# Kernel optimization log

Measured on AMD Instinct MI355X. Metric: run time of the kernel, lower is better.

Reference implementation:

```python
import jax, jax.numpy as jnp
import numpy as np

N_DELAYS = 512
N_SAMPLES = 2 ** 15  # 32768


def _interp_linear(x, out_size):
    # F.interpolate(mode='linear', align_corners=False) on [B, C, L]
    L = x.shape[-1]
    scale = L / out_size
    pos = (jnp.arange(out_size, dtype=jnp.float32) + 0.5) * scale - 0.5
    pos = jnp.clip(pos, 0.0, L - 1)
    i0 = jnp.floor(pos).astype(jnp.int32)
    i1 = jnp.minimum(i0 + 1, L - 1)
    w = (pos - i0).astype(x.dtype)
    return x[..., i0] * (1.0 - w) + x[..., i1] * w


def _interp_nearest(x, out_size):
    # F.interpolate(mode='nearest') on [B, C, L]: idx = floor(j * L/out)
    L = x.shape[-1]
    idx = jnp.clip(jnp.floor(jnp.arange(out_size) * (L / out_size)).astype(jnp.int32), 0, L - 1)
    return x[..., idx]


def setup_inputs() -> dict:
    key = jax.random.key(0)
    k1, k2, k3, k4, k5 = jax.random.split(key, 5)
    batch = 8
    impulse = jax.random.normal(k1, (batch, 128), dtype=jnp.float32)
    delay_selection = jax.random.normal(k2, (batch, N_DELAYS, 16), dtype=jnp.float32)
    damping = jax.random.normal(k3, (batch, 1), dtype=jnp.float32)
    filt = jax.random.normal(k4, (batch, 16), dtype=jnp.float32)
    # torch forward draws uniform(-1,1) noise; passed as input for determinism
    noise = jax.random.uniform(k5, (batch, 1, N_SAMPLES), dtype=jnp.float32, minval=-1.0, maxval=1.0)
    # comb-filter buffer: delays[i, ::i+1] = 1
    delays_np = np.zeros((N_DELAYS, N_SAMPLES), dtype=np.float32)
    for i in range(N_DELAYS):
        delays_np[i, ::i + 1] = 1.0
    delays = jnp.asarray(delays_np)
    return {"impulse": impulse, "delay_selection": delay_selection, "damping": damping,
            "filt": filt, "noise": noise, "delays": delays}


def reference(impulse, delay_selection, damping, filt, noise, delays):
    batch = delay_selection.shape[0]
    n_delays, n_samples = delays.shape
    n_frames = filt.shape[-1]

    # filter spectrum envelope: sigmoid -> linear upsample to n_samples//2 -> pad 1
    f = jax.nn.sigmoid(filt).reshape(-1, 1, n_frames)
    f = _interp_linear(f, n_samples // 2)
    filt_spec = jnp.pad(f, ((0, 0), (0, 0), (0, 1)))  # [B,1,n_samples//2+1]

    # impulse: squared envelope upsampled, modulating uniform noise
    imp = impulse.reshape(batch, 1, -1) ** 2
    imp = _interp_linear(imp, n_samples) * noise  # [B,1,n_samples]

    # damping: powers = linspace(1, 1, n_frames) == ones (faithful to source)
    damp = jax.nn.sigmoid(damping.reshape(batch, 1)) * 0.9999
    powers = jnp.linspace(1.0, float(damp.shape[-1]), n_frames)
    damp = damp[:, :, None] ** powers[None, None, :]  # [B,1,n_frames]
    damp = _interp_nearest(damp, n_samples)  # [B,1,n_samples]

    # sparse comb selection: softmax over delays, nearest upsample, weighted sum
    ds = jax.nn.softmax(delay_selection.reshape(batch, n_delays, -1), axis=1)
    ds = _interp_nearest(ds, n_samples)  # [B,n_delays,n_samples]
    d = jnp.einsum('bdn,dn->bn', ds, delays)[:, None, :] * damp  # [B,1,n_samples]

    # FFT convolution
    delay_spec = jnp.fft.rfft(d, axis=-1, norm='ortho')
    impulse_spec = jnp.fft.rfft(imp, axis=-1, norm='ortho')
    spec = delay_spec * impulse_spec * filt_spec
    final = jnp.fft.irfft(spec, n=n_samples, axis=-1, norm='ortho')
    return final
```

## Files before the change

kernel.cpp:

```cpp
#include <hip/hip_runtime.h>
#include <math.h>

#define NSAMP 32768
#define NDEL  512
#define NFR   16
#define BATCH 8
#define TWO_PI 6.283185307179586f

__device__ __forceinline__ float2 cmul(float2 a, float2 b) {
    return make_float2(a.x*b.x - a.y*b.y, a.x*b.y + a.y*b.x);
}
__device__ __forceinline__ float2 cadd(float2 a, float2 b){ return make_float2(a.x+b.x, a.y+b.y); }
__device__ __forceinline__ float2 csub(float2 a, float2 b){ return make_float2(a.x-b.x, a.y-b.y); }
__device__ __forceinline__ float2 crot(float2 z, float sign){ return make_float2(-sign*z.y, sign*z.x); }

__device__ __forceinline__ int phi(int i){ return i + (i >> 3); }

__device__ __forceinline__ void bfly8(const float2 v[8], float sign, float2 X[8]) {
    const float S2 = 0.70710678118654752f;
    float2 t0 = cadd(v[0], v[4]), t1 = csub(v[0], v[4]);
    float2 t2 = cadd(v[2], v[6]), t3 = crot(csub(v[2], v[6]), sign);
    float2 E0 = cadd(t0, t2), E1 = cadd(t1, t3), E2 = csub(t0, t2), E3 = csub(t1, t3);
    float2 u0 = cadd(v[1], v[5]), u1 = csub(v[1], v[5]);
    float2 u2 = cadd(v[3], v[7]), u3 = crot(csub(v[3], v[7]), sign);
    float2 O0 = cadd(u0, u2), O1 = cadd(u1, u3), O2 = csub(u0, u2), O3 = csub(u1, u3);
    float2 c1 = make_float2( S2, sign*S2);
    float2 c3 = make_float2(-S2, sign*S2);
    float2 w1o = cmul(c1, O1);
    float2 w2o = crot(O2, sign);
    float2 w3o = cmul(c3, O3);
    X[0]=cadd(E0,O0);  X[4]=csub(E0,O0);
    X[1]=cadd(E1,w1o); X[5]=csub(E1,w1o);
    X[2]=cadd(E2,w2o); X[6]=csub(E2,w2o);
    X[3]=cadd(E3,w3o); X[7]=csub(E3,w3o);
}

__device__ __forceinline__ void twiddle_q(float2 v[8], float ang1) {
    float sa, ca; __sincosf(ang1, &sa, &ca);
    float2 w1 = make_float2(ca, sa), wq = w1;
#pragma unroll
    for (int q = 1; q < 8; ++q) { v[q] = cmul(v[q], wq); wq = cmul(wq, w1); }
}

__global__ void build_kernel(const float* __restrict__ impulse,
                             const float* __restrict__ dsel,
                             const float* __restrict__ damping,
                             const float* __restrict__ noise,
                             float2* __restrict__ At) {
    const int b   = blockIdx.x >> 6;
    const int f   = (blockIdx.x >> 2) & 15;
    const int sub = blockIdx.x & 3;
    const int tid = threadIdx.x;
    __shared__ float Wrow[NDEL];
    __shared__ float dl[512];
    __shared__ float red[64];

    float v[8], m = -1e30f;
#pragma unroll
    for (int k = 0; k < 8; ++k) {
        v[k] = dsel[(b*NDEL + tid + 64*k)*NFR + f];
        m = fmaxf(m, v[k]);
    }
    red[tid] = m;
    __syncthreads();
    for (int off = 32; off > 0; off >>= 1) {
        if (tid < off) red[tid] = fmaxf(red[tid], red[tid+off]);
        __syncthreads();
    }
    float M = red[0];
    __syncthreads();
    float e[8], s = 0.0f;
#pragma unroll
    for (int k = 0; k < 8; ++k) { e[k] = expf(v[k] - M); s += e[k]; }
    red[tid] = s;
    __syncthreads();
    for (int off = 32; off > 0; off >>= 1) {
        if (tid < off) red[tid] += red[tid+off];
        __syncthreads();
    }
    float S = red[0];
    float damp = 1.0f/(1.0f + expf(-damping[b])) * 0.9999f;
    float scale = damp / S;
#pragma unroll
    for (int k = 0; k < 8; ++k) Wrow[tid + 64*k] = e[k] * scale;
    for (int k = tid; k < 512; k += 64) dl[k] = 0.0f;
    __syncthreads();

    const unsigned start = ((unsigned)f << 11) + ((unsigned)sub << 9);
    const float fstart = (float)start;

    for (unsigned t = 1; t < 64; ++t) {
        float wt = Wrow[t-1];
        unsigned q0 = (unsigned)(__fdividef(fstart, (float)t));
        unsigned n0 = q0 * t;
        while (n0 < start) n0 += t;
        while (n0 >= start + t) n0 -= t;
        for (unsigned i = (n0 - start) + (unsigned)tid * t; i < 512u; i += 64u * t)
            atomicAdd(&dl[i], wt);
    }
    for (unsigned t = 64u + (unsigned)tid; t <= 512u; t += 64u) {
        float wt = Wrow[t-1];
        unsigned q0 = (unsigned)(__fdividef(fstart, (float)t));
        unsigned n0 = q0 * t;
        while (n0 < start) n0 += t;
        while (n0 >= start + t) n0 -= t;
        for (unsigned i = n0 - start; i < 512u; i += t)
            atomicAdd(&dl[i], wt);
    }
    __syncthreads();

    const int n1base = (int)(start >> 6);
    float2* op = At + b*NSAMP + tid*512 + n1base;
#pragma unroll
    for (int q = 0; q < 8; ++q) {
        int n = (int)start + tid + 64*q;
        float pos = (n + 0.5f) * (1.0f/256.0f) - 0.5f;
        pos = fminf(fmaxf(pos, 0.0f), 127.0f);
        int i0 = (int)pos;
        float w = pos - (float)i0;
        int i1 = (i0 + 1 > 127) ? 127 : i0 + 1;
        float x0 = impulse[b*128 + i0]; x0 *= x0;
        float x1 = impulse[b*128 + i1]; x1 *= x1;
        float iv = (x0*(1.0f - w) + x1*w) * noise[b*NSAMP + n];
        op[q] = make_float2(dl[tid + 64*q], iv);
    }
}

__global__ void fft512_fwd_kernel(const float2* __restrict__ src,
                                  float2* __restrict__ dst) {
    const int j  = threadIdx.x;
    const int s  = blockIdx.x >> 6;
    const int n2 = blockIdx.x & 63;
    __shared__ float2 buf[2][576];
    const float sign = -1.0f;

    const float2* sp = src + s * NSAMP;
    float2 v[8], X[8];
#pragma unroll
    for (int q = 0; q < 8; ++q) v[q] = sp[n2*512 + j + 64*q];

    bfly8(v, sign, X);
#pragma unroll
    for (int r = 0; r < 8; ++r) buf[0][phi(8*j + r)] = X[r];
    __syncthreads();
#pragma unroll
    for (int q = 0; q < 8; ++q) v[q] = buf[0][phi(j + 64*q)];
    int jm = j & 7;
    twiddle_q(v, sign * TWO_PI * (float)jm * (1.0f/64.0f));
    bfly8(v, sign, X);
#pragma unroll
    for (int r = 0; r < 8; ++r) buf[1][phi(((j>>3)<<6) + jm + (r<<3))] = X[r];
    __syncthreads();
#pragma unroll
    for (int q = 0; q < 8; ++q) v[q] = buf[1][phi(j + 64*q)];
    twiddle_q(v, sign * TWO_PI * (float)j * (1.0f/512.0f));
    bfly8(v, sign, X);

    float2* dp = dst + s * NSAMP + n2 * 512;
#pragma unroll
    for (int r = 0; r < 8; ++r) {
        int k1 = j + 64*r;
        int pr = (n2 * k1) & (NSAMP - 1);
        float sa, ca; __sincosf(sign * TWO_PI * (float)pr * (1.0f/32768.0f), &sa, &ca);
        dp[k1] = cmul(X[r], make_float2(ca, sa));
    }
}

__global__ void mega_kernel(const float2* __restrict__ G,
                            float2* __restrict__ H,
                            const float* __restrict__ filt) {
    const int l  = threadIdx.x;
    const int cc = l & 7, jj = l >> 3;
    const int s  = blockIdx.x >> 6;
    const int g  = blockIdx.x & 63;
    __shared__ float2 Z[8][65];
    __shared__ float2 buf[576];
    __shared__ float fs[NFR];
    __shared__ int cols[8];

    if (l < NFR) fs[l] = 1.0f/(1.0f + expf(-filt[s*NFR + l]));
    if (l < 8) {
        int col;
        if (l < 4)        col = 4*g + l;
        else if (g == 0)  col = (l == 4) ? 256 : 512 - (l - 4);
        else              col = 512 - 4*g - (l - 4);
        cols[l] = col;
    }
    __syncthreads();

    const float2* sp = G + s * NSAMP;
    const int mycol = cols[cc];
    float2 v[8], X[8];

#pragma unroll
    for (int q = 0; q < 8; ++q) v[q] = sp[(jj + 8*q)*512 + mycol];
    bfly8(v, -1.0f, X);
#pragma unroll
    for (int r = 0; r < 8; ++r) buf[phi(cc*64 + jj*8 + r)] = X[r];
    __syncthreads();
#pragma unroll
    for (int q = 0; q < 8; ++q) v[q] = buf[phi(cc*64 + jj + 8*q)];
    twiddle_q(v, -TWO_PI * (float)jj * (1.0f/64.0f));
    bfly8(v, -1.0f, X);
#pragma unroll
    for (int r = 0; r < 8; ++r) Z[cc][jj + 8*r] = X[r];
    __syncthreads();

    const float SCALE = 1.0f / (32768.0f * 181.01933598375618f);
#pragma unroll
    for (int it = 0; it < 4; ++it) {
        int c  = l & 3;
        int k2 = (l >> 2) + 16*it;
        if (!(g == 0 && c == 0)) {
            int col = cols[c];
            float2 Zk = Z[c][k2];
            float2 Zr = Z[c+4][63 - k2];
            float2 Zrc = make_float2(Zr.x, -Zr.y);
            float2 D = make_float2(0.5f*(Zk.x + Zrc.x), 0.5f*(Zk.y + Zrc.y));
            float2 df = make_float2(Zk.x - Zrc.x, Zk.y - Zrc.y);
            float2 I = make_float2(0.5f*df.y, -0.5f*df.x);
            int k = col + 512*k2;
            int jjb = (k <= NSAMP - k) ? k : NSAMP - k;
            float fv = 0.0f;
            if (jjb < NSAMP/2) {
                float pos = (jjb + 0.5f) * (1.0f/1024.0f) - 0.5f;
                pos = fminf(fmaxf(pos, 0.0f), 15.0f);
                int i0 = (int)pos;
                float w = pos - (float)i0;
                int i1 = (i0 + 1 > 15) ? 15 : i0 + 1;
                fv = fs[i0]*(1.0f - w) + fs[i1]*w;
            }
            float2 spec = cmul(D, I);
            float gs = fv * SCALE;
            Z[c][k2]        = make_float2( spec.x*gs,  spec.y*gs);
            Z[c+4][63 - k2] = make_float2( spec.x*gs, -spec.y*gs);
        }
    }
    if (g == 0) {
        if (l <= 32) {
            int k2 = l, k2p = (64 - k2) & 63;
            float2 Zk = Z[0][k2];
            float2 Zr = Z[0][k2p];
            float2 Zrc = make_float2(Zr.x, -Zr.y);
            float2 D = make_float2(0.5f*(Zk.x + Zrc.x), 0.5f*(Zk.y + Zrc.y));
            float2 df = make_float2(Zk.x - Zrc.x, Zk.y - Zrc.y);
            float2 I = make_float2(0.5f*df.y, -0.5f*df.x);
            int k = 512*k2;
            int jjb = (k <= NSAMP - k) ? k : NSAMP - k;
            float fv = 0.0f;
            if (jjb < NSAMP/2) {
                float pos = (jjb + 0.5f) * (1.0f/1024.0f) - 0.5f;
                pos = fminf(fmaxf(pos, 0.0f), 15.0f);
                int i0 = (int)pos;
                float w = pos - (float)i0;
                int i1 = (i0 + 1 > 15) ? 15 : i0 + 1;
                fv = fs[i0]*(1.0f - w) + fs[i1]*w;
            }
            float2 spec = cmul(D, I);
            float gs = fv * SCALE;
            Z[0][k2]  = make_float2( spec.x*gs,  spec.y*gs);
            Z[0][k2p] = make_float2( spec.x*gs, -spec.y*gs);
        }
        if (l < 32) {
            int k2 = l, k2p = 63 - k2;
            float2 Zk = Z[4][k2];
            float2 Zr = Z[4][k2p];
            float2 Zrc = make_float2(Zr.x, -Zr.y);
            float2 D = make_float2(0.5f*(Zk.x + Zrc.x), 0.5f*(Zk.y + Zrc.y));
            float2 df = make_float2(Zk.x - Zrc.x, Zk.y - Zrc.y);
            float2 I = make_float2(0.5f*df.y, -0.5f*df.x);
            int k = 256 + 512*k2;
            int jjb = (k <= NSAMP - k) ? k : NSAMP - k;
            float fv = 0.0f;
            {
                float pos = (jjb + 0.5f) * (1.0f/1024.0f) - 0.5f;
                pos = fminf(fmaxf(pos, 0.0f), 15.0f);
                int i0 = (int)pos;
                float w = pos - (float)i0;
                int i1 = (i0 + 1 > 15) ? 15 : i0 + 1;
                fv = fs[i0]*(1.0f - w) + fs[i1]*w;
            }
            float2 spec = cmul(D, I);
            float gs = fv * SCALE;
            Z[4][k2]  = make_float2( spec.x*gs,  spec.y*gs);
            Z[4][k2p] = make_float2( spec.x*gs, -spec.y*gs);
        }
    }
    __syncthreads();

#pragma unroll
    for (int q = 0; q < 8; ++q) v[q] = Z[cc][jj + 8*q];
    bfly8(v, 1.0f, X);
#pragma unroll
    for (int r = 0; r < 8; ++r) buf[phi(cc*64 + jj*8 + r)] = X[r];
    __syncthreads();
#pragma unroll
    for (int q = 0; q < 8; ++q) v[q] = buf[phi(cc*64 + jj + 8*q)];
    twiddle_q(v, TWO_PI * (float)jj * (1.0f/64.0f));
    bfly8(v, 1.0f, X);

    float2* hp = H + s * NSAMP + mycol;
#pragma unroll
    for (int r = 0; r < 8; ++r) {
        int n2 = jj + 8*r;
        int pr = (n2 * mycol) & (NSAMP - 1);
        float sa, ca; __sincosf(TWO_PI * (float)pr * (1.0f/32768.0f), &sa, &ca);
        hp[n2*512] = cmul(X[r], make_float2(ca, sa));
    }
}

__global__ void fft512_out_kernel(const float2* __restrict__ H,
                                  float* __restrict__ out) {
    const int j  = threadIdx.x;
    const int s  = blockIdx.x >> 6;
    const int n2 = blockIdx.x & 63;
    __shared__ float2 buf[2][576];
    const float sign = 1.0f;

    const float2* sp = H + s * NSAMP;
    float2 v[8], X[8];
#pragma unroll
    for (int q = 0; q < 8; ++q) v[q] = sp[n2*512 + j + 64*q];

    bfly8(v, sign, X);
#pragma unroll
    for (int r = 0; r < 8; ++r) buf[0][phi(8*j + r)] = X[r];
    __syncthreads();
#pragma unroll
    for (int q = 0; q < 8; ++q) v[q] = buf[0][phi(j + 64*q)];
    int jm = j & 7;
    twiddle_q(v, sign * TWO_PI * (float)jm * (1.0f/64.0f));
    bfly8(v, sign, X);
#pragma unroll
    for (int r = 0; r < 8; ++r) buf[1][phi(((j>>3)<<6) + jm + (r<<3))] = X[r];
    __syncthreads();
#pragma unroll
    for (int q = 0; q < 8; ++q) v[q] = buf[1][phi(j + 64*q)];
    twiddle_q(v, sign * TWO_PI * (float)j * (1.0f/512.0f));
    bfly8(v, sign, X);

    float* op = out + s * NSAMP + n2;
#pragma unroll
    for (int r = 0; r < 8; ++r) op[64*j + 4096*r] = X[r].x;
}

extern "C" void kernel_launch(void* const* d_in, const int* in_sizes, int n_in,
                              void* d_out, int out_size, void* d_ws, size_t ws_size,
                              hipStream_t stream) {
    const float* impulse = (const float*)d_in[0];
    const float* dsel    = (const float*)d_in[1];
    const float* damping = (const float*)d_in[2];
    const float* filt    = (const float*)d_in[3];
    const float* noise   = (const float*)d_in[4];
    float* out = (float*)d_out;

    float2* A = (float2*)d_ws;
    float2* B = A + BATCH * NSAMP;

    build_kernel    <<<dim3(512), dim3(64), 0, stream>>>(impulse, dsel, damping, noise, A);
    fft512_fwd_kernel<<<dim3(512), dim3(64), 0, stream>>>(A, B);
    mega_kernel     <<<dim3(512), dim3(64), 0, stream>>>(B, A, filt);
    fft512_out_kernel<<<dim3(512), dim3(64), 0, stream>>>(A, out);
}
```

Measured before the change: 134.5 us.

## Fuse comb-signal build into first FFT pass with strided-column comb generation

Merges the build kernel and the first 512-point FFT pass into one kernel. Each block now builds the strided column (n = 64*l + 4096*q + n2) that its FFT consumes, which removes the workspace round-trip and one launch. The comb accumulation is reworked with modular arithmetic, using a constexpr table for delays with small odd parts and a per-thread loop for the rest. The full 16x512 softmax weight table is recomputed per block from unnormalised exp values, with normalisation applied afterwards. This trades extra redundant exp/softmax work and 32KB+ of shared memory per block, which may lower occupancy, for less global traffic.

New measurement: 171.3 us. 1.27x slower.

```diff
diff --git a/kernel.cpp b/kernel.cpp
--- a/kernel.cpp
+++ b/kernel.cpp
@@ -42,78 +42,24 @@
     for (int q = 1; q < 8; ++q) { v[q] = cmul(v[q], wq); wq = cmul(wq, w1); }
 }
 
-__global__ void build_kernel(const float* __restrict__ impulse,
-                             const float* __restrict__ dsel,
-                             const float* __restrict__ damping,
-                             const float* __restrict__ noise,
-                             float2* __restrict__ At) {
-    const int b   = blockIdx.x >> 6;
-    const int f   = (blockIdx.x >> 2) & 15;
-    const int sub = blockIdx.x & 3;
-    const int tid = threadIdx.x;
-    __shared__ float Wrow[NDEL];
-    __shared__ float dl[512];
-    __shared__ float red[64];
-
-    float v[8], m = -1e30f;
-#pragma unroll
-    for (int k = 0; k < 8; ++k) {
-        v[k] = dsel[(b*NDEL + tid + 64*k)*NFR + f];
-        m = fmaxf(m, v[k]);
-    }
-    red[tid] = m;
-    __syncthreads();
-    for (int off = 32; off > 0; off >>= 1) {
-        if (tid < off) red[tid] = fmaxf(red[tid], red[tid+off]);
-        __syncthreads();
-    }
-    float M = red[0];
-    __syncthreads();
-    float e[8], s = 0.0f;
-#pragma unroll
-    for (int k = 0; k < 8; ++k) { e[k] = expf(v[k] - M); s += e[k]; }
-    red[tid] = s;
-    __syncthreads();
-    for (int off = 32; off > 0; off >>= 1) {
-        if (tid < off) red[tid] += red[tid+off];
-        __syncthreads();
-    }
-    float S = red[0];
-    float damp = 1.0f/(1.0f + expf(-damping[b])) * 0.9999f;
-    float scale = damp / S;
-#pragma unroll
-    for (int k = 0; k < 8; ++k) Wrow[tid + 64*k] = e[k] * scale;
-    for (int k = tid; k < 512; k += 64) dl[k] = 0.0f;
-    __syncthreads();
-
-    const unsigned start = ((unsigned)f << 11) + ((unsigned)sub << 9);
-    const float fstart = (float)start;
-
-    for (unsigned t = 1; t < 64; ++t) {
-        float wt = Wrow[t-1];
-        unsigned q0 = (unsigned)(__fdividef(fstart, (float)t));
-        unsigned n0 = q0 * t;
-        while (n0 < start) n0 += t;
-        while (n0 >= start + t) n0 -= t;
-        for (unsigned i = (n0 - start) + (unsigned)tid * t; i < 512u; i += 64u * t)
-            atomicAdd(&dl[i], wt);
-    }
-    for (unsigned t = 64u + (unsigned)tid; t <= 512u; t += 64u) {
-        float wt = Wrow[t-1];
-        unsigned q0 = (unsigned)(__fdividef(fstart, (float)t));
-        unsigned n0 = q0 * t;
-        while (n0 < start) n0 += t;
-        while (n0 >= start + t) n0 -= t;
-        for (unsigned i = n0 - start; i < 512u; i += t)
-            atomicAdd(&dl[i], wt);
-    }
-    __syncthreads();
-
-    const int n1base = (int)(start >> 6);
-    float2* op = At + b*NSAMP + tid*512 + n1base;
+__global__ void build_fft_kernel(const float* __restrict__ impulse,
+                                 const float* __restrict__ dsel,
+                                 const float* __restrict__ damping,
+                                 const float* __restrict__ noise,
+                                 float2* __restrict__ G) {
+    const int l  = threadIdx.x;
+    const int b  = blockIdx.x >> 6;
+    const int n2 = blockIdx.x & 63;
+
+    __shared__ float  W[16*512];
+    __shared__ float  sc[16];
+    __shared__ float  dl[512];
+    __shared__ float2 buf[2][576];
+
+    float iv[8];
 #pragma unroll
     for (int q = 0; q < 8; ++q) {
-        int n = (int)start + tid + 64*q;
+        int n = 64*l + 4096*q + n2;
         float pos = (n + 0.5f) * (1.0f/256.0f) - 0.5f;
         pos = fminf(fmaxf(pos, 0.0f), 127.0f);
         int i0 = (int)pos;
@@ -121,48 +67,100 @@
         int i1 = (i0 + 1 > 127) ? 127 : i0 + 1;
         float x0 = impulse[b*128 + i0]; x0 *= x0;
         float x1 = impulse[b*128 + i1]; x1 *= x1;
-        float iv = (x0*(1.0f - w) + x1*w) * noise[b*NSAMP + n];
-        op[q] = make_float2(dl[tid + 64*q], iv);
-    }
-}
-
-__global__ void fft512_fwd_kernel(const float2* __restrict__ src,
-                                  float2* __restrict__ dst) {
-    const int j  = threadIdx.x;
-    const int s  = blockIdx.x >> 6;
-    const int n2 = blockIdx.x & 63;
-    __shared__ float2 buf[2][576];
+        iv[q] = (x0*(1.0f - w) + x1*w) * noise[b*NSAMP + n];
+    }
+
+    {
+        const int f   = l >> 2;
+        const int sub = l & 3;
+        const float* dp = dsel + b*NDEL*NFR;
+        float s = 0.0f;
+#pragma unroll 4
+        for (int i = 0; i < 128; ++i) {
+            int ti = sub + 4*i;
+            float e = __expf(dp[ti*NFR + f]);
+            W[(f << 9) + ti] = e;
+            s += e;
+        }
+        s += __shfl_xor(s, 1);
+        s += __shfl_xor(s, 2);
+        float damp = 0.9999f / (1.0f + __expf(-damping[b]));
+        if (sub == 0) sc[f] = damp / s;
+    }
+#pragma unroll
+    for (int q = 0; q < 8; ++q) dl[l + 64*q] = 0.0f;
+    __syncthreads();
+
+    {
+        constexpr int TA_t[32]  = {1,2,3,4,5,6,7,8,10,12,14,16,20,24,28,32,
+                                   40,48,56,64,80,96,112,128,160,192,224,256,320,384,448,512};
+        constexpr int TA_lg[32] = {0,1,0,2,0,1,0,3, 1, 2, 1, 4, 2, 3, 2, 5,
+                                    3, 4, 3, 6, 4, 5,  4,  6,  5,  6,  5,  6,  6,  6,  6,  6};
+        constexpr int TA_m[32]  = {1,1,3,1,5,3,7,1, 5, 3, 7, 1, 5, 3, 7, 1,
+                                    5, 3, 7, 1, 5, 3,  7,  2,  5,  3,  7,  4,  5,  6,  7,  8};
+#pragma unroll
+        for (int ii = 0; ii < 32; ++ii) {
+            const int t = TA_t[ii], lg = TA_lg[ii], m = TA_m[ii];
+            if ((n2 & ((1 << lg) - 1)) == 0) {
+                int r = (n2 >> lg) % m;
+                int x = (m - r) % m;
+#pragma unroll
+                for (int h = 0; h < 6 - lg; ++h)
+                    x = (x & 1) ? (x + m) >> 1 : x >> 1;
+                const float* wrow = W + (t - 1);
+                for (int n1 = x + l*m; n1 < 512; n1 += 64*m)
+                    atomicAdd(&dl[n1], wrow[(n1 >> 5) << 9]);
+            }
+        }
+    }
+    for (int t = l + 1; t <= 512; t += 64) {
+        int g = t & (-t); if (g > 64) g = 64;
+        int lg = __ffs(g) - 1;
+        int m = t >> lg;
+        if (m <= 8) continue;
+        if (n2 & (g - 1)) continue;
+        int r = n2 >> lg;
+        while (r >= m) r -= m;
+        int x = (r == 0) ? 0 : m - r;
+        int k = 6 - lg;
+        for (int h = 0; h < k; ++h) x = (x & 1) ? (x + m) >> 1 : x >> 1;
+        const float* wrow = W + (t - 1);
+        for (int n1 = x; n1 < 512; n1 += m)
+            atomicAdd(&dl[n1], wrow[(n1 >> 5) << 9]);
+    }
+    __syncthreads();
+
     const float sign = -1.0f;
-
-    const float2* sp = src + s * NSAMP;
     float2 v[8], X[8];
 #pragma unroll
-    for (int q = 0; q < 8; ++q) v[q] = sp[n2*512 + j + 64*q];
-
-    bfly8(v, sign, X);
-#pragma unroll
-    for (int r = 0; r < 8; ++r) buf[0][phi(8*j + r)] = X[r];
-    __syncthreads();
-#pragma unroll
-    for (int q = 0; q < 8; ++q) v[q] = buf[0][phi(j + 64*q)];
-    int jm = j & 7;
+    for (int q = 0; q < 8; ++q) {
+        int n1 = l + 64*q;
+        v[q] = make_float2(dl[n1] * sc[n1 >> 5], iv[q]);
+    }
+    bfly8(v, sign, X);
+#pragma unroll
+    for (int r = 0; r < 8; ++r) buf[0][phi(8*l + r)] = X[r];
+    __syncthreads();
+#pragma unroll
+    for (int q = 0; q < 8; ++q) v[q] = buf[0][phi(l + 64*q)];
+    int jm = l & 7;
     twiddle_q(v, sign * TWO_PI * (float)jm * (1.0f/64.0f));
     bfly8(v, sign, X);
 #pragma unroll
-    for (int r = 0; r < 8; ++r) buf[1][phi(((j>>3)<<6) + jm + (r<<3))] = X[r];
-    __syncthreads();
-#pragma unroll
-    for (int q = 0; q < 8; ++q) v[q] = buf[1][phi(j + 64*q)];
-    twiddle_q(v, sign * TWO_PI * (float)j * (1.0f/512.0f));
-    bfly8(v, sign, X);
-
-    float2* dp = dst + s * NSAMP + n2 * 512;
+    for (int r = 0; r < 8; ++r) buf[1][phi(((l>>3)<<6) + jm + (r<<3))] = X[r];
+    __syncthreads();
+#pragma unroll
+    for (int q = 0; q < 8; ++q) v[q] = buf[1][phi(l + 64*q)];
+    twiddle_q(v, sign * TWO_PI * (float)l * (1.0f/512.0f));
+    bfly8(v, sign, X);
+
+    float2* gp = G + b*NSAMP + n2*512;
 #pragma unroll
     for (int r = 0; r < 8; ++r) {
-        int k1 = j + 64*r;
+        int k1 = l + 64*r;
         int pr = (n2 * k1) & (NSAMP - 1);
         float sa, ca; __sincosf(sign * TWO_PI * (float)pr * (1.0f/32768.0f), &sa, &ca);
-        dp[k1] = cmul(X[r], make_float2(ca, sa));
+        gp[k1] = cmul(X[r], make_float2(ca, sa));
     }
 }
 
@@ -357,8 +355,7 @@
     float2* A = (float2*)d_ws;
     float2* B = A + BATCH * NSAMP;
 
-    build_kernel    <<<dim3(512), dim3(64), 0, stream>>>(impulse, dsel, damping, noise, A);
-    fft512_fwd_kernel<<<dim3(512), dim3(64), 0, stream>>>(A, B);
-    mega_kernel     <<<dim3(512), dim3(64), 0, stream>>>(B, A, filt);
-    fft512_out_kernel<<<dim3(512), dim3(64), 0, stream>>>(A, out);
-}
+    build_fft_kernel <<<dim3(512), dim3(64), 0, stream>>>(impulse, dsel, damping, noise, A);
+    mega_kernel      <<<dim3(512), dim3(64), 0, stream>>>(A, B, filt);
+    fft512_out_kernel<<<dim3(512), dim3(64), 0, stream>>>(B, out);
+}
```
